# Kernel optimization log

Measured on AMD Instinct MI355X. Metric: run time of the kernel, lower is better.

## Reference

```python
import jax, jax.numpy as jnp
import numpy as np

N_AGENTS = 512
OBS = 128          # embed_fc_input_size (args.obs_space)
INP = 656          # input_shape
HID = 64           # rnn_hidden_dim
LAT = 256          # latent_dim (hard-coded)
NH = 64            # NN_HIDDEN_SIZE (hard-coded)
VAR_FLOOR = 0.002
KL_W = 1e-4
H_W = 1e-4
SOFT_W = 1.0
BN_EPS = 1e-5
LOG2PI = float(np.log(2.0 * np.pi))


def _bn(x, g, b, axis):
    # BatchNorm1d in training mode: biased batch stats over `axis`
    m = x.mean(axis=axis, keepdims=True)
    v = x.var(axis=axis, keepdims=True)
    return g * (x - m) / jnp.sqrt(v + BN_EPS) + b


def setup_inputs() -> dict:
    key = jax.random.key(0)
    ks = jax.random.split(key, 12)
    s = 0.02  # small init so exp(log-var head) stays tame
    p = {}
    p["obs"] = jax.random.normal(ks[0], (N_AGENTS, INP), jnp.float32)
    p["hidden_state"] = jax.random.normal(ks[1], (N_AGENTS, HID), jnp.float32)
    p["eps"] = jax.random.normal(ks[2], (N_AGENTS, LAT), jnp.float32)

    def lin(k, din, dout):
        return jax.random.normal(k, (din, dout), jnp.float32) * s, jnp.zeros((dout,), jnp.float32)

    # embed_net: Linear(OBS,64) -> BN -> LeakyReLU -> Linear(64, 2*LAT)
    p["eW1"], p["eb1"] = lin(ks[3], OBS, NH)
    p["eg"], p["ebt"] = jnp.ones((NH,), jnp.float32), jnp.zeros((NH,), jnp.float32)
    p["eW2"], p["eb2"] = lin(ks[4], NH, 2 * LAT)
    # inference_net: Linear(HID+INP,64) -> BN -> LeakyReLU -> Linear(64, 2*LAT)
    p["iW1"], p["ib1"] = lin(ks[5], HID + INP, NH)
    p["ig"], p["ibt"] = jnp.ones((NH,), jnp.float32), jnp.zeros((NH,), jnp.float32)
    p["iW2"], p["ib2"] = lin(ks[6], NH, 2 * LAT)
    # dis_net: Linear(2*LAT,64) -> BN -> LeakyReLU -> Linear(64,1)
    p["dW1"], p["db1"] = lin(ks[7], 2 * LAT, NH)
    p["dg"], p["dbt"] = jnp.ones((NH,), jnp.float32), jnp.zeros((NH,), jnp.float32)
    p["dW2"], p["db2"] = lin(ks[8], NH, 1)
    return p


def reference(obs, hidden_state, eps,
              eW1, eb1, eg, ebt, eW2, eb2,
              iW1, ib1, ig, ibt, iW2, ib2,
              dW1, db1, dg, dbt, dW2, db2):
    n = N_AGENTS  # bs == 1 is hard-coded in the module
    # --- embed_net ---
    emb_in = obs[:, -OBS:]
    h = jax.nn.leaky_relu(_bn(emb_in @ eW1 + eb1, eg, ebt, axis=0))
    lat = h @ eW2 + eb2                       # [n, 2*LAT]
    mu = lat[:, :LAT]
    var = jnp.maximum(jnp.exp(lat[:, LAT:]), VAR_FLOOR)
    sig = jnp.sqrt(var)
    latent = mu + sig * eps                   # rsample

    # --- inference_net (h_in detached) ---
    inf_in = jnp.concatenate([jax.lax.stop_gradient(hidden_state), obs], axis=1)
    hi = jax.nn.leaky_relu(_bn(inf_in @ iW1 + ib1, ig, ibt, axis=0))
    li = hi @ iW2 + ib2
    mu_q = li[:, :LAT]
    var_q = jnp.maximum(jnp.exp(li[:, LAT:]), VAR_FLOOR)
    sig_q = jnp.sqrt(var_q)

    entropy = (0.5 + 0.5 * LOG2PI + jnp.log(sig)).sum(-1).mean()
    kl = (jnp.log(sig_q / sig) + (var + (mu - mu_q) ** 2) / (2.0 * var_q) - 0.5).sum(-1).mean()
    loss0 = jnp.minimum(entropy * H_W + kl * KL_W, 2000.0)
    ce_loss = jnp.log1p(jnp.exp(loss0))

    # --- vectorized ring-shift pairwise pass (replaces n_agents Python loop) ---
    shifts = jnp.arange(1, n + 1)                        # loop iterations 1..n
    idx = (jnp.arange(n)[None, :] - shifts[:, None]) % n  # [n_shifts, n]
    moved = latent[idx]                                   # [S, n, LAT]

    # mi: per-dim Normal(mu_j, sig_j).log_prob of shifted latents
    logp = -((moved - mu[None]) ** 2) / (2.0 * var[None]) - jnp.log(sig)[None] - 0.5 * LOG2PI
    mi = jnp.maximum(logp + 13.9, -13.9).sum(-1) / LAT    # [S, n]

    # dis_net on concat(latent_j, moved_{s,j}); BN stats per shift iteration (batch = n)
    pair = jnp.concatenate([jnp.broadcast_to(latent[None], (n, n, LAT)), moved], axis=-1)
    h1 = pair @ dW1 + db1                                 # [S, n, NH]
    h1 = jax.nn.leaky_relu(_bn(h1, dg, dbt, axis=1))
    dis = jnp.abs(h1 @ dW2 + db2)[..., 0]                 # [S, n]

    mi_cat = mi.reshape(1, -1)                            # shift-major, matches cat order
    dis_cat = dis.reshape(1, -1)

    mi_n = (mi_cat - mi_cat.min(1, keepdims=True)) / (mi_cat.max(1, keepdims=True) - mi_cat.min(1, keepdims=True) + 1e-12)
    dis_n = (dis_cat - dis_cat.min(1, keepdims=True)) / (dis_cat.max(1, keepdims=True) - dis_cat.min(1, keepdims=True) + 1e-12)

    dis_loss = -jnp.minimum(mi_n + dis_n, 1.0).sum() / n  # / bs / n_agents, bs=1
    dis_norm = jnp.abs(dis_n).sum(axis=1).sum() / n
    c_dis_loss = (dis_norm + SOFT_W * dis_loss) / n
    loss = ce_loss + c_dis_loss
    return loss, c_dis_loss, ce_loss
```

## Files before the change

kernel.cpp:

```cpp
#include <hip/hip_runtime.h>

#define LOG2PI_F 1.8378770664093453f

#define W_ENC_PRE 0
#define W_INF_PRE 32768
#define W_FIN     65792
#define W_MIMM    65796
#define W_DSMM    66308
#define W_ENT     67332
#define W_KL      67588
#define W_LATENT  67844
#define W_RPC     198916
#define W_A       723204
#define W_B       755972
#define W_AT      788740
#define W_BT      821508
#define W_ALPHA   854276
#define W_BETA    887044
#define W_MI      919812
#define W_DIS     1181956
#define W_PACC    1446144

__global__ __launch_bounds__(256) void k_pre(
    const float* __restrict__ obs, const float* __restrict__ hid,
    const float* __restrict__ eW1, const float* __restrict__ iW1,
    float* __restrict__ enc_pre, float* __restrict__ inf_pre,
    float* __restrict__ pacc) {
  __shared__ float x[2][720];
  __shared__ float pi[4][2][64];
  __shared__ float pe[4][2][64];
  __shared__ float sb[256];
  const int t = threadIdx.x;
  const int vb = blockIdx.x;
  const int i0 = vb * 2;
#pragma unroll
  for (int r = 0; r < 2; ++r)
    for (int k = t; k < 720; k += 256)
      x[r][k] = (k < 64) ? hid[(i0 + r) * 64 + k] : obs[(i0 + r) * 656 + (k - 64)];
  __syncthreads();
  const int c = t & 63, q = t >> 6;
  {
    float a0 = 0.f, a1 = 0.f;
    const int k0 = q * 180;
    for (int k = k0; k < k0 + 180; ++k) {
      const float w = iW1[k * 64 + c];
      a0 = fmaf(x[0][k], w, a0);
      a1 = fmaf(x[1][k], w, a1);
    }
    pi[q][0][c] = a0;
    pi[q][1][c] = a1;
  }
  {
    float a0 = 0.f, a1 = 0.f;
    const int k0 = q * 32;
    for (int k = k0; k < k0 + 32; ++k) {
      const float w = eW1[k * 64 + c];
      a0 = fmaf(x[0][592 + k], w, a0);
      a1 = fmaf(x[1][592 + k], w, a1);
    }
    pe[q][0][c] = a0;
    pe[q][1][c] = a1;
  }
  __syncthreads();
  float s;
  if (t < 128) {
    const int r = t >> 6, c2 = t & 63;
    s = pi[0][r][c2] + pi[1][r][c2] + pi[2][r][c2] + pi[3][r][c2];
    inf_pre[(i0 + r) * 64 + c2] = s;
  } else {
    const int r = (t >> 6) & 1, c2 = t & 63;
    s = pe[0][r][c2] + pe[1][r][c2] + pe[2][r][c2] + pe[3][r][c2];
    enc_pre[(i0 + r) * 64 + c2] = s;
  }
  sb[t] = s;
  __syncthreads();
  if (t < 64) {
    const float e0 = sb[128 + t], e1 = sb[192 + t];
    pacc[vb * 256 + t] = e0 + e1;
    pacc[vb * 256 + 64 + t] = e0 * e0 + e1 * e1;
  } else if (t < 128) {
    const int c2 = t - 64;
    const float v0 = sb[c2], v1 = sb[64 + c2];
    pacc[vb * 256 + 128 + c2] = v0 + v1;
    pacc[vb * 256 + 192 + c2] = v0 * v0 + v1 * v1;
  }
}

__global__ __launch_bounds__(256) void k_lat(
    const float* __restrict__ enc_pre, const float* __restrict__ inf_pre,
    const float* __restrict__ pacc, const float* __restrict__ eg,
    const float* __restrict__ ebt, const float* __restrict__ ig,
    const float* __restrict__ ibt, const float* __restrict__ eW2,
    const float* __restrict__ eb2, const float* __restrict__ iW2,
    const float* __restrict__ ib2, const float* __restrict__ eps,
    float* __restrict__ latent, float* __restrict__ rpc,
    float* __restrict__ ent_part, float* __restrict__ kl_part) {
  __shared__ float sval[256];
  __shared__ float sc[2][64], sh[2][64];
  __shared__ float h[2][2][64];
  __shared__ float red[256];
  const int t = threadIdx.x;
  const int i0 = blockIdx.x * 2;
  {
    float v = 0.f;
    for (int b = 0; b < 256; ++b) v += pacc[b * 256 + t];
    sval[t] = v;
  }
  __syncthreads();
  if (t < 128) {
    const int w = t >> 6, c = t & 63;
    const float sum = sval[w * 128 + c], sq = sval[w * 128 + 64 + c];
    const float mean = sum * (1.f / 512.f);
    float var = sq * (1.f / 512.f) - mean * mean;
    var = fmaxf(var, 0.f);
    const float g = w ? ig[c] : eg[c];
    const float bt = w ? ibt[c] : ebt[c];
    const float scale = g * rsqrtf(var + 1e-5f);
    sc[w][c] = scale;
    sh[w][c] = bt - mean * scale;
  }
  __syncthreads();
  {
    const int w = t >> 7, r = (t >> 6) & 1, c = t & 63;
    const float* pre = w ? inf_pre : enc_pre;
    const float v = fmaf(pre[(i0 + r) * 64 + c], sc[w][c], sh[w][c]);
    h[w][r][c] = (v >= 0.f) ? v : 0.01f * v;
  }
  __syncthreads();
  float me[2] = {0.f, 0.f}, ve[2] = {0.f, 0.f};
  float mq[2] = {0.f, 0.f}, vq[2] = {0.f, 0.f};
  for (int c = 0; c < 64; ++c) {
    const float we1 = eW2[c * 512 + t], we2 = eW2[c * 512 + 256 + t];
    const float wi1 = iW2[c * 512 + t], wi2 = iW2[c * 512 + 256 + t];
#pragma unroll
    for (int r = 0; r < 2; ++r) {
      me[r] = fmaf(h[0][r][c], we1, me[r]);
      ve[r] = fmaf(h[0][r][c], we2, ve[r]);
      mq[r] = fmaf(h[1][r][c], wi1, mq[r]);
      vq[r] = fmaf(h[1][r][c], wi2, vq[r]);
    }
  }
  const float ebm = eb2[t], ebv = eb2[256 + t];
  const float ibm = ib2[t], ibv = ib2[256 + t];
  float ent_l = 0.f, kl_l = 0.f;
#pragma unroll
  for (int r = 0; r < 2; ++r) {
    const int i = i0 + r;
    const float m = me[r] + ebm;
    const float var = fmaxf(expf(ve[r] + ebv), 0.002f);
    const float lse = 0.5f * logf(var);
    const float sig = sqrtf(var);
    const float mqq = mq[r] + ibm;
    const float varq = fmaxf(expf(vq[r] + ibv), 0.002f);
    const float lsq = 0.5f * logf(varq);
    latent[i * 256 + t] = fmaf(sig, eps[i * 256 + t], m);
    const float r_ = sqrtf(0.5f / var);
    float4 o;
    o.x = r_;
    o.y = m * r_;
    o.z = 13.9f - 0.5f * LOG2PI_F - lse;
    o.w = 0.f;
    *(float4*)&rpc[(i * 256 + t) * 4] = o;
    ent_l += 0.5f + 0.5f * LOG2PI_F + lse;
    const float dmu = m - mqq;
    kl_l += lsq - lse + (var + dmu * dmu) * (0.5f / varq) - 0.5f;
  }
  red[t] = ent_l;
  __syncthreads();
  for (int o = 128; o; o >>= 1) {
    if (t < o) red[t] += red[t + o];
    __syncthreads();
  }
  if (t == 0) ent_part[blockIdx.x] = red[0];
  __syncthreads();
  red[t] = kl_l;
  __syncthreads();
  for (int o = 128; o; o >>= 1) {
    if (t < o) red[t] += red[t + o];
    __syncthreads();
  }
  if (t == 0) kl_part[blockIdx.x] = red[0];
}

__global__ __launch_bounds__(256) void k_AB(
    const float* __restrict__ latent, const float* __restrict__ dW1,
    float* __restrict__ A, float* __restrict__ B, float* __restrict__ At,
    float* __restrict__ Bt, float* __restrict__ fin) {
  if (blockIdx.x == 0 && threadIdx.x == 0) {
    fin[0] = 0.f;
    fin[1] = 0.f;
    ((unsigned*)fin)[2] = 0u;
  }
  __shared__ float ls[2][256];
  __shared__ float pA[4][2][64], pB[4][2][64];
  const int t = threadIdx.x;
  const int j0 = blockIdx.x * 2;
  ls[0][t] = latent[j0 * 256 + t];
  ls[1][t] = latent[(j0 + 1) * 256 + t];
  __syncthreads();
  const int c = t & 63, q = t >> 6;
  float aA0 = 0.f, aA1 = 0.f, aB0 = 0.f, aB1 = 0.f;
  const int k0 = q * 64;
  for (int k = k0; k < k0 + 64; ++k) {
    const float wA = dW1[k * 64 + c];
    const float wB = dW1[(256 + k) * 64 + c];
    aA0 = fmaf(ls[0][k], wA, aA0);
    aA1 = fmaf(ls[1][k], wA, aA1);
    aB0 = fmaf(ls[0][k], wB, aB0);
    aB1 = fmaf(ls[1][k], wB, aB1);
  }
  pA[q][0][c] = aA0;
  pA[q][1][c] = aA1;
  pB[q][0][c] = aB0;
  pB[q][1][c] = aB1;
  __syncthreads();
  if (t < 128) {
    const int r = t >> 6, c2 = t & 63;
    const float s = pA[0][r][c2] + pA[1][r][c2] + pA[2][r][c2] + pA[3][r][c2];
    A[(j0 + r) * 64 + c2] = s;
    At[c2 * 512 + j0 + r] = s;
  } else {
    const int r = (t >> 6) & 1, c2 = t & 63;
    const float s = pB[0][r][c2] + pB[1][r][c2] + pB[2][r][c2] + pB[3][r][c2];
    B[(j0 + r) * 64 + c2] = s;
    Bt[c2 * 512 + j0 + r] = s;
  }
}

__global__ __launch_bounds__(256) void k_cross(
    const float* __restrict__ At, const float* __restrict__ Bt,
    const float* __restrict__ dg, const float* __restrict__ dbt,
    float* __restrict__ alpha, float* __restrict__ beta) {
  __shared__ float a[512], bb[512];
  __shared__ float red[256];
  __shared__ float pc[4][64];
  const int t = threadIdx.x;
  const int c = blockIdx.x >> 3;
  const int s0 = (blockIdx.x & 7) * 64;
  const float a0 = At[c * 512 + t], a1 = At[c * 512 + 256 + t];
  const float b0 = Bt[c * 512 + t], b1 = Bt[c * 512 + 256 + t];
  a[t] = a0;
  a[t + 256] = a1;
  bb[t] = b0;
  bb[t + 256] = b1;
  red[t] = a0 + a1 + b0 + b1;
  __syncthreads();
  for (int o = 128; o; o >>= 1) {
    if (t < o) red[t] += red[t + o];
    __syncthreads();
  }
  const float S = red[0];
  __syncthreads();
  red[t] = a0 * a0 + a1 * a1 + b0 * b0 + b1 * b1;
  __syncthreads();
  for (int o = 128; o; o >>= 1) {
    if (t < o) red[t] += red[t + o];
    __syncthreads();
  }
  const float Q = red[0];
  const int sl = t & 63, part = t >> 6;
  const int s = s0 + sl;
  float cr = 0.f;
  for (int j = part * 128; j < part * 128 + 128; ++j)
    cr = fmaf(a[j], bb[(j - s - 1) & 511], cr);
  pc[part][sl] = cr;
  __syncthreads();
  if (t < 64) {
    const int ss = s0 + t;
    const float cross = pc[0][t] + pc[1][t] + pc[2][t] + pc[3][t];
    const float mean = S * (1.f / 512.f);
    const float var = (Q + 2.f * cross) * (1.f / 512.f) - mean * mean;
    const float gc = dg[c], bc = dbt[c];
    const float al = rsqrtf(var + 1e-5f) * gc;
    alpha[ss * 64 + c] = al;
    beta[ss * 64 + c] = bc - mean * al;
  }
}

__global__ __launch_bounds__(256) void k_midis(
    const float* __restrict__ latent, const float* __restrict__ rpc,
    const float* __restrict__ A, const float* __restrict__ B,
    const float* __restrict__ alpha, const float* __restrict__ beta,
    const float* __restrict__ dW2, const float* __restrict__ db2,
    float* __restrict__ mi, float* __restrict__ dis,
    float2* __restrict__ miMM, float2* __restrict__ dsMM) {
  __shared__ __align__(16) float sm[15276];
  const int t = threadIdx.x;
  if (blockIdx.x < 256) {
    float* lats = sm;
    float* rpcs = sm + 4160;
    float* mt = sm + 8256;
    float* fmn = sm + 9344;
    float* fmx = sm + 9600;
    const int vb = blockIdx.x;
    const int jt = vb & 31, pt = vb >> 5;
    const int j0 = jt * 16, p0 = pt * 64;
    const int pl = t & 31, jg = t >> 5;
    float regL[16], regR[16];
#pragma unroll
    for (int i = 0; i < 16; ++i) {
      const int idx = t + i * 256;
      regL[i] = latent[(p0 + (idx >> 6)) * 256 + (idx & 63)];
      regR[i] = rpc[(j0 + (idx >> 8)) * 1024 + (idx & 255)];
    }
    float a00 = 0.f, a01 = 0.f, a10 = 0.f, a11 = 0.f;
    for (int kc = 0; kc < 4; ++kc) {
      __syncthreads();
#pragma unroll
      for (int i = 0; i < 16; ++i) {
        const int idx = t + i * 256;
        lats[(idx >> 6) * 65 + (idx & 63)] = regL[i];
        rpcs[idx] = regR[i];
      }
      __syncthreads();
      if (kc < 3) {
#pragma unroll
        for (int i = 0; i < 16; ++i) {
          const int idx = t + i * 256;
          regL[i] = latent[(p0 + (idx >> 6)) * 256 + (kc + 1) * 64 + (idx & 63)];
          regR[i] = rpc[(j0 + (idx >> 8)) * 1024 + (kc + 1) * 256 + (idx & 255)];
        }
      }
      const float4* rp0 = (const float4*)&rpcs[(jg * 2) * 256];
      const float4* rp1 = (const float4*)&rpcs[(jg * 2 + 1) * 256];
#pragma unroll 8
      for (int k = 0; k < 64; ++k) {
        const float l0 = lats[pl * 65 + k], l1 = lats[(pl + 32) * 65 + k];
        const float4 r0 = rp0[k];
        const float4 r1 = rp1[k];
        float v;
        v = fmaf(l0, r0.x, -r0.y);
        a00 += fmaxf(fmaf(-v, v, r0.z), -13.9f);
        v = fmaf(l1, r0.x, -r0.y);
        a01 += fmaxf(fmaf(-v, v, r0.z), -13.9f);
        v = fmaf(l0, r1.x, -r1.y);
        a10 += fmaxf(fmaf(-v, v, r1.z), -13.9f);
        v = fmaf(l1, r1.x, -r1.y);
        a11 += fmaxf(fmaf(-v, v, r1.z), -13.9f);
      }
    }
    a00 *= (1.f / 256.f);
    a01 *= (1.f / 256.f);
    a10 *= (1.f / 256.f);
    a11 *= (1.f / 256.f);
    __syncthreads();
    mt[pl * 17 + jg * 2] = a00;
    mt[(pl + 32) * 17 + jg * 2] = a01;
    mt[pl * 17 + jg * 2 + 1] = a10;
    mt[(pl + 32) * 17 + jg * 2 + 1] = a11;
    fmn[t] = fminf(fminf(a00, a01), fminf(a10, a11));
    fmx[t] = fmaxf(fmaxf(a00, a01), fmaxf(a10, a11));
    __syncthreads();
    for (int o = 128; o; o >>= 1) {
      if (t < o) {
        fmn[t] = fminf(fmn[t], fmn[t + o]);
        fmx[t] = fmaxf(fmx[t], fmx[t + o]);
      }
      __syncthreads();
    }
    if (t == 0) miMM[vb] = make_float2(fmn[0], fmx[0]);
    for (int i = t; i < 1024; i += 256) {
      const int pr = i >> 4, jc = i & 15;
      mi[(p0 + pr) * 512 + (j0 + jc)] = mt[pr * 17 + jc];
    }
  } else {
    float* As = sm;
    float* Bs = sm + 528;
    float* als = sm + 4752;
    float* bes = sm + 9438;
    float* w2s = sm + 14124;
    float* dt = sm + 14188;
    float* fmn = sm + 14764;
    float* fmx = sm + 15020;
    const int vb = blockIdx.x - 256;
    const int jt = vb & 63, pt = vb >> 6;
    const int j0 = jt * 8, p0 = pt * 64;
    for (int idx = t; idx < 8 * 64; idx += 256)
      As[(idx >> 6) * 66 + (idx & 63)] = A[(j0 + (idx >> 6)) * 64 + (idx & 63)];
    for (int idx = t; idx < 64 * 64; idx += 256)
      Bs[(idx >> 6) * 66 + (idx & 63)] = B[(p0 + (idx >> 6)) * 64 + (idx & 63)];
    for (int idx = t; idx < 71 * 64; idx += 256) {
      const int r = idx >> 6, c = idx & 63;
      const int s = (j0 - p0 - 64 + r) & 511;
      als[r * 66 + c] = alpha[s * 64 + c];
      bes[r * 66 + c] = beta[s * 64 + c];
    }
    if (t < 64) w2s[t] = dW2[t];
    const float db2v = db2[0];
    __syncthreads();
    const int pl = t & 31, jg = t >> 5;
    const int rb0 = jg - pl + 63;
    const int rb1 = jg - pl + 31;
    float acc0 = 0.f, acc1 = 0.f;
    for (int c = 0; c < 64; c += 2) {
      const float2 av = *(const float2*)&As[jg * 66 + c];
      const float2 bv0 = *(const float2*)&Bs[pl * 66 + c];
      const float2 bv1 = *(const float2*)&Bs[(pl + 32) * 66 + c];
      const float2 al0 = *(const float2*)&als[rb0 * 66 + c];
      const float2 al1 = *(const float2*)&als[rb1 * 66 + c];
      const float2 be0 = *(const float2*)&bes[rb0 * 66 + c];
      const float2 be1 = *(const float2*)&bes[rb1 * 66 + c];
      const float2 w = *(const float2*)&w2s[c];
      float v;
      v = fmaf(av.x + bv0.x, al0.x, be0.x);
      v = (v >= 0.f) ? v : 0.01f * v;
      acc0 = fmaf(v, w.x, acc0);
      v = fmaf(av.y + bv0.y, al0.y, be0.y);
      v = (v >= 0.f) ? v : 0.01f * v;
      acc0 = fmaf(v, w.y, acc0);
      v = fmaf(av.x + bv1.x, al1.x, be1.x);
      v = (v >= 0.f) ? v : 0.01f * v;
      acc1 = fmaf(v, w.x, acc1);
      v = fmaf(av.y + bv1.y, al1.y, be1.y);
      v = (v >= 0.f) ? v : 0.01f * v;
      acc1 = fmaf(v, w.y, acc1);
    }
    acc0 = fabsf(acc0 + db2v);
    acc1 = fabsf(acc1 + db2v);
    dt[pl * 9 + jg] = acc0;
    dt[(pl + 32) * 9 + jg] = acc1;
    fmn[t] = fminf(acc0, acc1);
    fmx[t] = fmaxf(acc0, acc1);
    __syncthreads();
    for (int o = 128; o; o >>= 1) {
      if (t < o) {
        fmn[t] = fminf(fmn[t], fmn[t + o]);
        fmx[t] = fmaxf(fmx[t], fmx[t + o]);
      }
      __syncthreads();
    }
    if (t == 0) dsMM[vb] = make_float2(fmn[0], fmx[0]);
    for (int idx = t; idx < 512; idx += 256) {
      const int pr = idx >> 3, jc = idx & 7;
      dis[(p0 + pr) * 512 + (j0 + jc)] = dt[pr * 9 + jc];
    }
  }
}

__global__ __launch_bounds__(256) void k_sumfin(
    const float* __restrict__ mi, const float* __restrict__ dis,
    const float2* __restrict__ miMM, const float2* __restrict__ dsMM,
    float* __restrict__ fin, const float* __restrict__ ent_part,
    const float* __restrict__ kl_part, float* __restrict__ out) {
  __shared__ float red1[256], red2[256], red3[256], red4[256];
  __shared__ int lastflag;
  const int t = threadIdx.x;
  {
    const float2 v = miMM[t];
    const float2 w0 = dsMM[t], w1 = dsMM[t + 256];
    red1[t] = v.x;
    red2[t] = v.y;
    red3[t] = fminf(w0.x, w1.x);
    red4[t] = fmaxf(w0.y, w1.y);
  }
  __syncthreads();
  for (int o = 128; o; o >>= 1) {
    if (t < o) {
      red1[t] = fminf(red1[t], red1[t + o]);
      red2[t] = fmaxf(red2[t], red2[t + o]);
      red3[t] = fminf(red3[t], red3[t + o]);
      red4[t] = fmaxf(red4[t], red4[t + o]);
    }
    __syncthreads();
  }
  const float mi_mn = red1[0], mi_mx = red2[0];
  const float d_mn = red3[0], d_mx = red4[0];
  __syncthreads();
  const float inv_mi = 1.f / (mi_mx - mi_mn + 1e-12f);
  const float inv_d = 1.f / (d_mx - d_mn + 1e-12f);
  float s1 = 0.f, s2 = 0.f;
  for (int i = blockIdx.x * 256 + t; i < 512 * 512; i += 65536) {
    const float mn_ = (mi[i] - mi_mn) * inv_mi;
    const float dn_ = (dis[i] - d_mn) * inv_d;
    s1 += fminf(mn_ + dn_, 1.0f);
    s2 += dn_;
  }
  red1[t] = s1;
  red2[t] = s2;
  __syncthreads();
  for (int o = 128; o; o >>= 1) {
    if (t < o) {
      red1[t] += red1[t + o];
      red2[t] += red2[t + o];
    }
    __syncthreads();
  }
  if (t == 0) {
    atomicAdd(&fin[0], red1[0]);
    atomicAdd(&fin[1], red2[0]);
    __threadfence();
    const unsigned old = atomicAdd((unsigned*)&fin[2], 1u);
    lastflag = (old == 255u) ? 1 : 0;
  }
  __syncthreads();
  if (!lastflag) return;
  red1[t] = ent_part[t];
  red2[t] = kl_part[t];
  __syncthreads();
  for (int o = 128; o; o >>= 1) {
    if (t < o) {
      red1[t] += red1[t + o];
      red2[t] += red2[t + o];
    }
    __syncthreads();
  }
  if (t == 0) {
    const float S1 = atomicAdd(&fin[0], 0.f);
    const float S2 = atomicAdd(&fin[1], 0.f);
    const double entropy = (double)red1[0] / 512.0;
    const double kl = (double)red2[0] / 512.0;
    double l0 = entropy * 1e-4 + kl * 1e-4;
    if (l0 > 2000.0) l0 = 2000.0;
    const double ce = log1p(exp(l0));
    const double dis_loss = -(double)S1 / 512.0;
    const double dis_norm = (double)S2 / 512.0;
    const double c_dis = (dis_norm + dis_loss) / 512.0;
    out[0] = (float)(ce + c_dis);
    out[1] = (float)c_dis;
    out[2] = (float)ce;
  }
}

extern "C" void kernel_launch(void* const* d_in, const int* in_sizes, int n_in,
                              void* d_out, int out_size, void* d_ws,
                              size_t ws_size, hipStream_t stream) {
  (void)in_sizes;
  (void)n_in;
  (void)out_size;
  (void)ws_size;
  const float* obs = (const float*)d_in[0];
  const float* hid = (const float*)d_in[1];
  const float* eps = (const float*)d_in[2];
  const float* eW1 = (const float*)d_in[3];
  const float* eg = (const float*)d_in[5];
  const float* ebt = (const float*)d_in[6];
  const float* eW2 = (const float*)d_in[7];
  const float* eb2 = (const float*)d_in[8];
  const float* iW1 = (const float*)d_in[9];
  const float* ig = (const float*)d_in[11];
  const float* ibt = (const float*)d_in[12];
  const float* iW2 = (const float*)d_in[13];
  const float* ib2 = (const float*)d_in[14];
  const float* dW1 = (const float*)d_in[15];
  const float* dg = (const float*)d_in[17];
  const float* dbt = (const float*)d_in[18];
  const float* dW2 = (const float*)d_in[19];
  const float* db2 = (const float*)d_in[20];
  float* ws = (float*)d_ws;
  float* out = (float*)d_out;

  k_pre<<<256, 256, 0, stream>>>(obs, hid, eW1, iW1, ws + W_ENC_PRE,
                                 ws + W_INF_PRE, ws + W_PACC);
  k_lat<<<256, 256, 0, stream>>>(ws + W_ENC_PRE, ws + W_INF_PRE, ws + W_PACC,
                                 eg, ebt, ig, ibt, eW2, eb2, iW2, ib2, eps,
                                 ws + W_LATENT, ws + W_RPC, ws + W_ENT,
                                 ws + W_KL);
  k_AB<<<256, 256, 0, stream>>>(ws + W_LATENT, dW1, ws + W_A, ws + W_B,
                                ws + W_AT, ws + W_BT, ws + W_FIN);
  k_cross<<<512, 256, 0, stream>>>(ws + W_AT, ws + W_BT, dg, dbt, ws + W_ALPHA,
                                   ws + W_BETA);
  k_midis<<<768, 256, 0, stream>>>(ws + W_LATENT, ws + W_RPC, ws + W_A,
                                   ws + W_B, ws + W_ALPHA, ws + W_BETA, dW2,
                                   db2, ws + W_MI, ws + W_DIS,
                                   (float2*)(ws + W_MIMM),
                                   (float2*)(ws + W_DSMM));
  k_sumfin<<<256, 256, 0, stream>>>(ws + W_MI, ws + W_DIS,
                                    (const float2*)(ws + W_MIMM),
                                    (const float2*)(ws + W_DSMM), ws + W_FIN,
                                    ws + W_ENT, ws + W_KL, out);
}
```

Baseline: 184.7 us.

## Fuse latent and dis-net projection kernels, interleave midis blocks, vectorise final sum

Merges k_lat and k_AB into one kernel, so each block keeps its two latent rows in shared memory and computes the dW1 projections directly. This removes one launch and a global round trip of the latent tensor. In k_midis the MI and dis blocks are interleaved by block index to balance work across CUs. The final normalised-sum loop in k_sumfin now reads float4 once per thread instead of striding in a loop, which assumes exactly 256 blocks cover the 512x512 arrays.

Result: slower. 191.5 us (+3.7%).

```diff
diff --git a/kernel.cpp b/kernel.cpp
--- a/kernel.cpp
+++ b/kernel.cpp
@@ -86,21 +86,30 @@
   }
 }
 
-__global__ __launch_bounds__(256) void k_lat(
+__global__ __launch_bounds__(256) void k_latAB(
     const float* __restrict__ enc_pre, const float* __restrict__ inf_pre,
     const float* __restrict__ pacc, const float* __restrict__ eg,
     const float* __restrict__ ebt, const float* __restrict__ ig,
     const float* __restrict__ ibt, const float* __restrict__ eW2,
     const float* __restrict__ eb2, const float* __restrict__ iW2,
     const float* __restrict__ ib2, const float* __restrict__ eps,
-    float* __restrict__ latent, float* __restrict__ rpc,
-    float* __restrict__ ent_part, float* __restrict__ kl_part) {
+    const float* __restrict__ dW1, float* __restrict__ latent,
+    float* __restrict__ rpc, float* __restrict__ ent_part,
+    float* __restrict__ kl_part, float* __restrict__ A, float* __restrict__ B,
+    float* __restrict__ At, float* __restrict__ Bt, float* __restrict__ fin) {
   __shared__ float sval[256];
   __shared__ float sc[2][64], sh[2][64];
   __shared__ float h[2][2][64];
   __shared__ float red[256];
+  __shared__ float ls[2][256];
+  __shared__ float pA[4][2][64], pB[4][2][64];
   const int t = threadIdx.x;
   const int i0 = blockIdx.x * 2;
+  if (blockIdx.x == 0 && t == 0) {
+    fin[0] = 0.f;
+    fin[1] = 0.f;
+    ((unsigned*)fin)[2] = 0u;
+  }
   {
     float v = 0.f;
     for (int b = 0; b < 256; ++b) v += pacc[b * 256 + t];
@@ -143,6 +152,7 @@
   const float ebm = eb2[t], ebv = eb2[256 + t];
   const float ibm = ib2[t], ibv = ib2[256 + t];
   float ent_l = 0.f, kl_l = 0.f;
+  float latv[2];
 #pragma unroll
   for (int r = 0; r < 2; ++r) {
     const int i = i0 + r;
@@ -153,7 +163,8 @@
     const float mqq = mq[r] + ibm;
     const float varq = fmaxf(expf(vq[r] + ibv), 0.002f);
     const float lsq = 0.5f * logf(varq);
-    latent[i * 256 + t] = fmaf(sig, eps[i * 256 + t], m);
+    latv[r] = fmaf(sig, eps[i * 256 + t], m);
+    latent[i * 256 + t] = latv[r];
     const float r_ = sqrtf(0.5f / var);
     float4 o;
     o.x = r_;
@@ -166,6 +177,8 @@
     kl_l += lsq - lse + (var + dmu * dmu) * (0.5f / varq) - 0.5f;
   }
   red[t] = ent_l;
+  ls[0][t] = latv[0];
+  ls[1][t] = latv[1];
   __syncthreads();
   for (int o = 128; o; o >>= 1) {
     if (t < o) red[t] += red[t + o];
@@ -180,25 +193,8 @@
     __syncthreads();
   }
   if (t == 0) kl_part[blockIdx.x] = red[0];
-}
-
-__global__ __launch_bounds__(256) void k_AB(
-    const float* __restrict__ latent, const float* __restrict__ dW1,
-    float* __restrict__ A, float* __restrict__ B, float* __restrict__ At,
-    float* __restrict__ Bt, float* __restrict__ fin) {
-  if (blockIdx.x == 0 && threadIdx.x == 0) {
-    fin[0] = 0.f;
-    fin[1] = 0.f;
-    ((unsigned*)fin)[2] = 0u;
-  }
-  __shared__ float ls[2][256];
-  __shared__ float pA[4][2][64], pB[4][2][64];
-  const int t = threadIdx.x;
-  const int j0 = blockIdx.x * 2;
-  ls[0][t] = latent[j0 * 256 + t];
-  ls[1][t] = latent[(j0 + 1) * 256 + t];
-  __syncthreads();
   const int c = t & 63, q = t >> 6;
+  const int j0 = i0;
   float aA0 = 0.f, aA1 = 0.f, aB0 = 0.f, aB1 = 0.f;
   const int k0 = q * 64;
   for (int k = k0; k < k0 + 64; ++k) {
@@ -286,13 +282,14 @@
     float2* __restrict__ miMM, float2* __restrict__ dsMM) {
   __shared__ __align__(16) float sm[15276];
   const int t = threadIdx.x;
-  if (blockIdx.x < 256) {
+  const bool is_mi = (blockIdx.x < 512) && ((blockIdx.x & 1) == 0);
+  if (is_mi) {
     float* lats = sm;
     float* rpcs = sm + 4160;
     float* mt = sm + 8256;
     float* fmn = sm + 9344;
     float* fmx = sm + 9600;
-    const int vb = blockIdx.x;
+    const int vb = blockIdx.x >> 1;
     const int jt = vb & 31, pt = vb >> 5;
     const int j0 = jt * 16, p0 = pt * 64;
     const int pl = t & 31, jg = t >> 5;
@@ -372,7 +369,8 @@
     float* dt = sm + 14188;
     float* fmn = sm + 14764;
     float* fmx = sm + 15020;
-    const int vb = blockIdx.x - 256;
+    const int vb = (blockIdx.x < 512) ? (int)(blockIdx.x >> 1)
+                                      : (int)(blockIdx.x - 256);
     const int jt = vb & 63, pt = vb >> 6;
     const int j0 = jt * 8, p0 = pt * 64;
     for (int idx = t; idx < 8 * 64; idx += 256)
@@ -469,9 +467,25 @@
   const float inv_mi = 1.f / (mi_mx - mi_mn + 1e-12f);
   const float inv_d = 1.f / (d_mx - d_mn + 1e-12f);
   float s1 = 0.f, s2 = 0.f;
-  for (int i = blockIdx.x * 256 + t; i < 512 * 512; i += 65536) {
-    const float mn_ = (mi[i] - mi_mn) * inv_mi;
-    const float dn_ = (dis[i] - d_mn) * inv_d;
+  {
+    const int idx = blockIdx.x * 256 + t;
+    const float4 m4 = ((const float4*)mi)[idx];
+    const float4 d4 = ((const float4*)dis)[idx];
+    float mn_, dn_;
+    mn_ = (m4.x - mi_mn) * inv_mi;
+    dn_ = (d4.x - d_mn) * inv_d;
+    s1 += fminf(mn_ + dn_, 1.0f);
+    s2 += dn_;
+    mn_ = (m4.y - mi_mn) * inv_mi;
+    dn_ = (d4.y - d_mn) * inv_d;
+    s1 += fminf(mn_ + dn_, 1.0f);
+    s2 += dn_;
+    mn_ = (m4.z - mi_mn) * inv_mi;
+    dn_ = (d4.z - d_mn) * inv_d;
+    s1 += fminf(mn_ + dn_, 1.0f);
+    s2 += dn_;
+    mn_ = (m4.w - mi_mn) * inv_mi;
+    dn_ = (d4.w - d_mn) * inv_d;
     s1 += fminf(mn_ + dn_, 1.0f);
     s2 += dn_;
   }
@@ -551,12 +565,11 @@
 
   k_pre<<<256, 256, 0, stream>>>(obs, hid, eW1, iW1, ws + W_ENC_PRE,
                                  ws + W_INF_PRE, ws + W_PACC);
-  k_lat<<<256, 256, 0, stream>>>(ws + W_ENC_PRE, ws + W_INF_PRE, ws + W_PACC,
-                                 eg, ebt, ig, ibt, eW2, eb2, iW2, ib2, eps,
-                                 ws + W_LATENT, ws + W_RPC, ws + W_ENT,
-                                 ws + W_KL);
-  k_AB<<<256, 256, 0, stream>>>(ws + W_LATENT, dW1, ws + W_A, ws + W_B,
-                                ws + W_AT, ws + W_BT, ws + W_FIN);
+  k_latAB<<<256, 256, 0, stream>>>(ws + W_ENC_PRE, ws + W_INF_PRE, ws + W_PACC,
+                                   eg, ebt, ig, ibt, eW2, eb2, iW2, ib2, eps,
+                                   dW1, ws + W_LATENT, ws + W_RPC, ws + W_ENT,
+                                   ws + W_KL, ws + W_A, ws + W_B, ws + W_AT,
+                                   ws + W_BT, ws + W_FIN);
   k_cross<<<512, 256, 0, stream>>>(ws + W_AT, ws + W_BT, dg, dbt, ws + W_ALPHA,
                                    ws + W_BETA);
   k_midis<<<768, 256, 0, stream>>>(ws + W_LATENT, ws + W_RPC, ws + W_A,
```
